# Optimization experiments

Measured on AMD Instinct MI355X. Metric: run time of the kernel, lower is better.

## Reference

```python
import jax, jax.numpy as jnp
import numpy as np

NU = 0.01 / np.pi  # Burgers viscosity
LAYERS = [2, 128, 128, 128, 128, 1]
N_EQ, N_INIT, N_BND = 131072, 4096, 4096


def setup_inputs() -> dict:
    key = jax.random.key(0)
    ks = jax.random.split(key, 16)
    inp = {
        'tx_equation': jax.random.uniform(ks[0], (N_EQ, 2), dtype=jnp.float32),
        'tx_init': jax.random.uniform(ks[1], (N_INIT, 2), dtype=jnp.float32),
        'tx_bound': jax.random.uniform(ks[2], (N_BND, 2), dtype=jnp.float32),
    }
    # Glorot-normal initialized Dense weights, zero biases (keras defaults in build_network)
    for i, (fin, fout) in enumerate(zip(LAYERS[:-1], LAYERS[1:])):
        std = np.sqrt(2.0 / (fin + fout)).astype(np.float32)
        inp[f'W{i}'] = jax.random.normal(ks[3 + i], (fin, fout), dtype=jnp.float32) * std
        inp[f'b{i}'] = jnp.zeros((fout,), dtype=jnp.float32)
    return inp


def _mlp_scalar(tx, Ws, bs):
    # tx: (2,) -> scalar u. tanh hidden layers, linear output.
    h = tx
    for W, b in zip(Ws[:-1], bs[:-1]):
        h = jnp.tanh(h @ W + b)
    return (h @ Ws[-1] + bs[-1])[0]


def reference(tx_equation, tx_init, tx_bound, W0, b0, W1, b1, W2, b2, W3, b3, W4, b4):
    Ws = [W0, W1, W2, W3, W4]
    bs = [b0, b1, b2, b3, b4]

    def u_s(tx):
        return _mlp_scalar(tx, Ws, bs)

    def u_x_s(tx):
        return jax.grad(u_s)(tx)[1]

    # PDE residual on collocation points
    u = jax.vmap(u_s)(tx_equation)                     # (N,)
    g = jax.vmap(jax.grad(u_s))(tx_equation)           # (N, 2) -> columns (u_t, u_x)
    u_t, u_x = g[:, 0], g[:, 1]
    u_xx = jax.vmap(jax.grad(u_x_s))(tx_equation)[:, 1]  # (N,)
    burgers_eq = (u_t + u * u_x - NU * u_xx)[:, None]     # (N, 1)

    # Initial / boundary predictions (single fused batch like tf.concat in call)
    tx_ib = jnp.concatenate([tx_init, tx_bound], axis=0)
    u_ib = jax.vmap(u_s)(tx_ib)[:, None]
    n_i = tx_init.shape[0]
    return burgers_eq, u_ib[:n_i], u_ib[n_i:]
```

## Files before the change

kernel.cpp:

```cpp
#include <hip/hip_runtime.h>
#include <math.h>

#define NU_F 0.0031830988618379067f
#define HS 136

typedef __attribute__((ext_vector_type(8))) _Float16 half8;
typedef __attribute__((ext_vector_type(4))) _Float16 half4;
typedef __attribute__((ext_vector_type(16))) float f32x16;

__device__ __forceinline__ float fast_tanh(float x) {
    const float e = __builtin_amdgcn_exp2f(x * 2.8853900817779268f);
    const float r = __builtin_amdgcn_rcpf(e + 1.f);
    return fmaf(-2.f, r, 1.f);
}

__global__ void prep_kernel(const float* __restrict__ W1,
                            const float* __restrict__ W2,
                            const float* __restrict__ W3,
                            _Float16* __restrict__ ws)
{
    const int g = blockIdx.x * 256 + threadIdx.x;
    const int l = g >> 14;
    const int r = g & 16383;
    const int n = r & 127;
    const int k = r >> 7;
    const float* W = (l == 0) ? W1 : (l == 1) ? W2 : W3;
    const float w = W[k * 128 + n];
    ws[l * 16384 + (k >> 4) * 2048 + n * 16 + (k & 15)] = (_Float16)w;
}

__launch_bounds__(256, 6)
__global__ void pinn_kernel(const float* __restrict__ tx_eq,
                            const float* __restrict__ tx_init,
                            const float* __restrict__ tx_bnd,
                            const float* __restrict__ W0, const float* __restrict__ b0,
                            const float* __restrict__ b1, const float* __restrict__ b2,
                            const float* __restrict__ b3,
                            const float* __restrict__ W4, const float* __restrict__ b4,
                            const _Float16* __restrict__ wt,
                            float* __restrict__ out)
{
    __shared__ _Float16 Hh[64][HS];

    const int tid   = threadIdx.x;
    const int blk   = blockIdx.x;
    const bool is_eq = (blk < 8192);
    const int w     = tid >> 6;
    const int lane  = tid & 63;
    const int col   = lane & 31;
    const int khalf = lane >> 5;
    const int ncol  = 32 * w + col;
    const int wofs  = ncol * 16 + khalf * 8;

    if (is_eq) {
        const int p  = tid >> 4;
        const int f0 = (tid & 15) * 8;
        const float tv = tx_eq[blk * 32 + 2 * p];
        const float xv = tx_eq[blk * 32 + 2 * p + 1];
        float vch[4][8];
        #pragma unroll
        for (int j = 0; j < 8; ++j) {
            const int f = f0 + j;
            const float w0v = W0[f];
            const float w1v = W0[128 + f];
            const float z = fmaf(tv, w0v, fmaf(xv, w1v, b0[f]));
            const float a = fast_tanh(z);
            const float s = 1.f - a * a;
            vch[0][j] = a;
            vch[1][j] = s * w0v;
            vch[2][j] = s * w1v;
            vch[3][j] = -2.f * a * s * w1v * w1v;
        }
        const int m0 = 4 * p;
        #pragma unroll
        for (int c = 0; c < 4; ++c) {
            half8 hh;
            #pragma unroll
            for (int j = 0; j < 8; ++j) hh[j] = (_Float16)vch[c][j];
            *(half8*)&Hh[m0 + c][f0] = hh;
        }
    } else {
        const int p  = tid >> 2;
        const int f0 = (tid & 3) * 32;
        const int gp = (blk - 8192) * 64 + p;
        const float* src = (gp < 4096) ? tx_init : tx_bnd;
        const int idx = (gp < 4096) ? gp : gp - 4096;
        const float tv = src[2 * idx];
        const float xv = src[2 * idx + 1];
        #pragma unroll
        for (int g = 0; g < 4; ++g) {
            half8 hh;
            #pragma unroll
            for (int j = 0; j < 8; ++j) {
                const int f = f0 + 8 * g + j;
                hh[j] = (_Float16)fast_tanh(fmaf(tv, W0[f], fmaf(xv, W0[128 + f], b0[f])));
            }
            *(half8*)&Hh[p][f0 + 8 * g] = hh;
        }
    }
    __syncthreads();

    const float* barr[3] = {b1, b2, b3};

    #pragma unroll 1
    for (int layer = 0; layer < 3; ++layer) {
        const _Float16* __restrict__ ph = wt + layer * 16384 + wofs;
        const float bias = barr[layer][ncol];

        half8 q0 = *(const half8*)(ph);
        half8 q1 = *(const half8*)(ph + 2048);
        half8 q2 = *(const half8*)(ph + 4096);
        half8 q3 = *(const half8*)(ph + 6144);
        half8 q4 = *(const half8*)(ph + 8192);
        half8 q5 = *(const half8*)(ph + 10240);
        half8 q6 = *(const half8*)(ph + 12288);
        half8 q7 = *(const half8*)(ph + 14336);

        f32x16 acc0, acc1;
        #pragma unroll
        for (int e = 0; e < 16; ++e) { acc0[e] = 0.f; acc1[e] = 0.f; }

#define KSTEP(KT, Q)                                                          \
        {                                                                     \
            const int k0 = KT * 16 + khalf * 8;                               \
            const half8 ah0 = *(const half8*)&Hh[col][k0];                    \
            const half8 ah1 = *(const half8*)&Hh[32 + col][k0];               \
            acc0 = __builtin_amdgcn_mfma_f32_32x32x16_f16(ah0, Q, acc0, 0, 0, 0); \
            acc1 = __builtin_amdgcn_mfma_f32_32x32x16_f16(ah1, Q, acc1, 0, 0, 0); \
        }
        KSTEP(0, q0) KSTEP(1, q1) KSTEP(2, q2) KSTEP(3, q3)
        KSTEP(4, q4) KSTEP(5, q5) KSTEP(6, q6) KSTEP(7, q7)
#undef KSTEP

        half4 h16[2][4];
        #pragma unroll
        for (int mt = 0; mt < 2; ++mt)
            #pragma unroll
            for (int g = 0; g < 4; ++g) {
                const float A0 = (mt ? acc1 : acc0)[4 * g + 0];
                const float A1 = (mt ? acc1 : acc0)[4 * g + 1];
                const float A2 = (mt ? acc1 : acc0)[4 * g + 2];
                const float A3 = (mt ? acc1 : acc0)[4 * g + 3];
                half4 hv;
                if (is_eq) {
                    const float a = fast_tanh(A0 + bias);
                    const float s = 1.f - a * a;
                    hv[0] = (_Float16)a;
                    hv[1] = (_Float16)(s * A1);
                    hv[2] = (_Float16)(s * A2);
                    hv[3] = (_Float16)fmaf(s, A3, -2.f * a * s * A2 * A2);
                } else {
                    hv[0] = (_Float16)fast_tanh(A0 + bias);
                    hv[1] = (_Float16)fast_tanh(A1 + bias);
                    hv[2] = (_Float16)fast_tanh(A2 + bias);
                    hv[3] = (_Float16)fast_tanh(A3 + bias);
                }
                h16[mt][g] = hv;
            }

        __syncthreads();

        #pragma unroll
        for (int mt = 0; mt < 2; ++mt)
            #pragma unroll
            for (int g = 0; g < 4; ++g) {
                const int mrow0 = mt * 32 + 8 * g + 4 * khalf;
                Hh[mrow0 + 0][ncol] = h16[mt][g][0];
                Hh[mrow0 + 1][ncol] = h16[mt][g][1];
                Hh[mrow0 + 2][ncol] = h16[mt][g][2];
                Hh[mrow0 + 3][ncol] = h16[mt][g][3];
            }
        __syncthreads();
    }

    {
        const float b4v = b4[0];
        const int m = tid >> 2;
        const int q = tid & 3;
        float dot = 0.f;
        #pragma unroll
        for (int g = 0; g < 4; ++g) {
            const int f = 32 * q + 8 * g;
            const half8 hh = *(const half8*)&Hh[m][f];
            const float4 wa = *(const float4*)&W4[f];
            const float4 wb = *(const float4*)&W4[f + 4];
            dot = fmaf((float)hh[0], wa.x, dot);
            dot = fmaf((float)hh[1], wa.y, dot);
            dot = fmaf((float)hh[2], wa.z, dot);
            dot = fmaf((float)hh[3], wa.w, dot);
            dot = fmaf((float)hh[4], wb.x, dot);
            dot = fmaf((float)hh[5], wb.y, dot);
            dot = fmaf((float)hh[6], wb.z, dot);
            dot = fmaf((float)hh[7], wb.w, dot);
        }
        dot += __shfl_xor(dot, 1);
        dot += __shfl_xor(dot, 2);

        if (is_eq) {
            const float uu   = __shfl(dot, (lane & 48) + 0)  + b4v;
            const float utv  = __shfl(dot, (lane & 48) + 4);
            const float uxv  = __shfl(dot, (lane & 48) + 8);
            const float uxxv = __shfl(dot, (lane & 48) + 12);
            if ((lane & 15) == 0)
                out[blk * 16 + 4 * w + (lane >> 4)] = fmaf(uu, uxv, utv) - NU_F * uxxv;
        } else {
            if (q == 0)
                out[131072 + (blk - 8192) * 64 + m] = dot + b4v;
        }
    }
}

extern "C" void kernel_launch(void* const* d_in, const int* in_sizes, int n_in,
                              void* d_out, int out_size, void* d_ws, size_t ws_size,
                              hipStream_t stream)
{
    const float* tx_eq   = (const float*)d_in[0];
    const float* tx_init = (const float*)d_in[1];
    const float* tx_bnd  = (const float*)d_in[2];
    const float* W0 = (const float*)d_in[3];
    const float* b0 = (const float*)d_in[4];
    const float* W1 = (const float*)d_in[5];
    const float* b1 = (const float*)d_in[6];
    const float* W2 = (const float*)d_in[7];
    const float* b2 = (const float*)d_in[8];
    const float* W3 = (const float*)d_in[9];
    const float* b3 = (const float*)d_in[10];
    const float* W4 = (const float*)d_in[11];
    const float* b4 = (const float*)d_in[12];
    float* out = (float*)d_out;
    _Float16* wt = (_Float16*)d_ws;

    hipLaunchKernelGGL(prep_kernel, dim3(192), dim3(256), 0, stream, W1, W2, W3, wt);
    hipLaunchKernelGGL(pinn_kernel, dim3(8320), dim3(256), 0, stream,
                       tx_eq, tx_init, tx_bnd, W0, b0, b1, b2, b3, W4, b4,
                       (const _Float16*)wt, out);
}
```

Baseline: 171.2 us.

## Split MFMA tile as 2x2 M/N per wave and relax launch bounds

Changes the per-wave work split from one 32-column N strip over both 32-row M halves to a 32-row M half by two 32-column N tiles. Each wave now loads one A fragment per k-step from LDS and reuses it for two MFMAs, halving LDS reads of activations, while loading twice as many weight fragments from global/L2 into registers. Launch bounds drop the minimum blocks per CU from 6 to 4 to make room for the extra weight registers, which may reduce occupancy.

```diff
diff --git a/kernel.cpp b/kernel.cpp
--- a/kernel.cpp
+++ b/kernel.cpp
@@ -29,7 +29,7 @@
     ws[l * 16384 + (k >> 4) * 2048 + n * 16 + (k & 15)] = (_Float16)w;
 }
 
-__launch_bounds__(256, 6)
+__launch_bounds__(256, 4)
 __global__ void pinn_kernel(const float* __restrict__ tx_eq,
                             const float* __restrict__ tx_init,
                             const float* __restrict__ tx_bnd,
@@ -49,8 +49,12 @@
     const int lane  = tid & 63;
     const int col   = lane & 31;
     const int khalf = lane >> 5;
-    const int ncol  = 32 * w + col;
-    const int wofs  = ncol * 16 + khalf * 8;
+    const int mhalf = w >> 1;
+    const int nhalf = w & 1;
+    const int n0    = 64 * nhalf + col;
+    const int n1    = n0 + 32;
+    const int arow  = 32 * mhalf + col;
+    const int wofs  = n0 * 16 + khalf * 8;
 
     if (is_eq) {
         const int p  = tid >> 4;
@@ -105,71 +109,83 @@
     #pragma unroll 1
     for (int layer = 0; layer < 3; ++layer) {
         const _Float16* __restrict__ ph = wt + layer * 16384 + wofs;
-        const float bias = barr[layer][ncol];
-
-        half8 q0 = *(const half8*)(ph);
-        half8 q1 = *(const half8*)(ph + 2048);
-        half8 q2 = *(const half8*)(ph + 4096);
-        half8 q3 = *(const half8*)(ph + 6144);
-        half8 q4 = *(const half8*)(ph + 8192);
-        half8 q5 = *(const half8*)(ph + 10240);
-        half8 q6 = *(const half8*)(ph + 12288);
-        half8 q7 = *(const half8*)(ph + 14336);
+        const float bias0 = barr[layer][n0];
+        const float bias1 = barr[layer][n1];
+
+        half8 qa0 = *(const half8*)(ph);
+        half8 qb0 = *(const half8*)(ph + 512);
+        half8 qa1 = *(const half8*)(ph + 2048);
+        half8 qb1 = *(const half8*)(ph + 2560);
+        half8 qa2 = *(const half8*)(ph + 4096);
+        half8 qb2 = *(const half8*)(ph + 4608);
+        half8 qa3 = *(const half8*)(ph + 6144);
+        half8 qb3 = *(const half8*)(ph + 6656);
+        half8 qa4 = *(const half8*)(ph + 8192);
+        half8 qb4 = *(const half8*)(ph + 8704);
+        half8 qa5 = *(const half8*)(ph + 10240);
+        half8 qb5 = *(const half8*)(ph + 10752);
+        half8 qa6 = *(const half8*)(ph + 12288);
+        half8 qb6 = *(const half8*)(ph + 12800);
+        half8 qa7 = *(const half8*)(ph + 14336);
+        half8 qb7 = *(const half8*)(ph + 14848);
 
         f32x16 acc0, acc1;
         #pragma unroll
         for (int e = 0; e < 16; ++e) { acc0[e] = 0.f; acc1[e] = 0.f; }
 
-#define KSTEP(KT, Q)                                                          \
+#define KSTEP(KT, QA, QB)                                                     \
         {                                                                     \
             const int k0 = KT * 16 + khalf * 8;                               \
-            const half8 ah0 = *(const half8*)&Hh[col][k0];                    \
-            const half8 ah1 = *(const half8*)&Hh[32 + col][k0];               \
-            acc0 = __builtin_amdgcn_mfma_f32_32x32x16_f16(ah0, Q, acc0, 0, 0, 0); \
-            acc1 = __builtin_amdgcn_mfma_f32_32x32x16_f16(ah1, Q, acc1, 0, 0, 0); \
-        }
-        KSTEP(0, q0) KSTEP(1, q1) KSTEP(2, q2) KSTEP(3, q3)
-        KSTEP(4, q4) KSTEP(5, q5) KSTEP(6, q6) KSTEP(7, q7)
+            const half8 ah = *(const half8*)&Hh[arow][k0];                    \
+            acc0 = __builtin_amdgcn_mfma_f32_32x32x16_f16(ah, QA, acc0, 0, 0, 0); \
+            acc1 = __builtin_amdgcn_mfma_f32_32x32x16_f16(ah, QB, acc1, 0, 0, 0); \
+        }
+        KSTEP(0, qa0, qb0) KSTEP(1, qa1, qb1) KSTEP(2, qa2, qb2) KSTEP(3, qa3, qb3)
+        KSTEP(4, qa4, qb4) KSTEP(5, qa5, qb5) KSTEP(6, qa6, qb6) KSTEP(7, qa7, qb7)
 #undef KSTEP
 
         half4 h16[2][4];
         #pragma unroll
-        for (int mt = 0; mt < 2; ++mt)
+        for (int a = 0; a < 2; ++a) {
+            const float bias = a ? bias1 : bias0;
             #pragma unroll
             for (int g = 0; g < 4; ++g) {
-                const float A0 = (mt ? acc1 : acc0)[4 * g + 0];
-                const float A1 = (mt ? acc1 : acc0)[4 * g + 1];
-                const float A2 = (mt ? acc1 : acc0)[4 * g + 2];
-                const float A3 = (mt ? acc1 : acc0)[4 * g + 3];
+                const float A0 = (a ? acc1 : acc0)[4 * g + 0];
+                const float A1 = (a ? acc1 : acc0)[4 * g + 1];
+                const float A2 = (a ? acc1 : acc0)[4 * g + 2];
+                const float A3 = (a ? acc1 : acc0)[4 * g + 3];
                 half4 hv;
                 if (is_eq) {
-                    const float a = fast_tanh(A0 + bias);
-                    const float s = 1.f - a * a;
-                    hv[0] = (_Float16)a;
+                    const float t = fast_tanh(A0 + bias);
+                    const float s = 1.f - t * t;
+                    hv[0] = (_Float16)t;
                     hv[1] = (_Float16)(s * A1);
                     hv[2] = (_Float16)(s * A2);
-                    hv[3] = (_Float16)fmaf(s, A3, -2.f * a * s * A2 * A2);
+                    hv[3] = (_Float16)fmaf(s, A3, -2.f * t * s * A2 * A2);
                 } else {
                     hv[0] = (_Float16)fast_tanh(A0 + bias);
                     hv[1] = (_Float16)fast_tanh(A1 + bias);
                     hv[2] = (_Float16)fast_tanh(A2 + bias);
                     hv[3] = (_Float16)fast_tanh(A3 + bias);
                 }
-                h16[mt][g] = hv;
+                h16[a][g] = hv;
             }
+        }
 
         __syncthreads();
 
         #pragma unroll
-        for (int mt = 0; mt < 2; ++mt)
+        for (int a = 0; a < 2; ++a) {
+            const int nc = a ? n1 : n0;
             #pragma unroll
             for (int g = 0; g < 4; ++g) {
-                const int mrow0 = mt * 32 + 8 * g + 4 * khalf;
-                Hh[mrow0 + 0][ncol] = h16[mt][g][0];
-                Hh[mrow0 + 1][ncol] = h16[mt][g][1];
-                Hh[mrow0 + 2][ncol] = h16[mt][g][2];
-                Hh[mrow0 + 3][ncol] = h16[mt][g][3];
+                const int mrow0 = 32 * mhalf + 8 * g + 4 * khalf;
+                Hh[mrow0 + 0][nc] = h16[a][g][0];
+                Hh[mrow0 + 1][nc] = h16[a][g][1];
+                Hh[mrow0 + 2][nc] = h16[a][g][2];
+                Hh[mrow0 + 3][nc] = h16[a][g][3];
             }
+        }
         __syncthreads();
     }
 
```

Result: slower. 182.4 us (+6.5%).
